# Performance work log

Measured on AMD Instinct MI355X. Metric: run time of the kernel, lower is better.

## Reference

```python
import jax, jax.numpy as jnp
import numpy as np
from jax.scipy.special import logsumexp, gammaln

B, T, D, K = 2048, 512, 64, 16  # num_sequences, max_length, data_dim (tones), hidden_dim per factor


def setup_inputs() -> dict:
    key = jax.random.key(0)
    k0, k1, k2, k3, k4 = jax.random.split(key, 5)
    sequences = jax.random.randint(k0, (B, T, D), 0, 2).astype(jnp.int32)  # binary piano-roll obs
    lengths = jax.random.randint(k1, (B,), 1, T + 1).astype(jnp.int32)
    probs_w = jax.nn.softmax(jax.random.normal(k2, (K, K), dtype=jnp.float32), axis=-1)  # row-stochastic
    probs_x = jax.nn.softmax(jax.random.normal(k3, (K, K), dtype=jnp.float32), axis=-1)
    probs_y = jax.random.uniform(k4, (K, K, D), dtype=jnp.float32) * 0.98 + 0.01  # in (0.01, 0.99)
    return {"sequences": sequences, "lengths": lengths,
            "probs_w": probs_w, "probs_x": probs_x, "probs_y": probs_y}


def _dirichlet_logpdf_rows(p, conc):
    # sum over rows of Dirichlet(conc_row).log_prob(p_row)
    return (((conc - 1.0) * jnp.log(p)).sum()
            + gammaln(conc.sum(-1)).sum() - gammaln(conc).sum())


def _log_joint(sequences, lengths, probs_w, probs_x, probs_y):
    dt = probs_y.dtype
    logTw = jnp.log(probs_w)            # (K, K) transition for w factor
    logTx = jnp.log(probs_x)            # (K, K) transition for x factor
    lp = jnp.log(probs_y)               # (K, K, D)
    l1p = jnp.log1p(-probs_y)           # (K, K, D)
    Wemit = (lp - l1p).reshape(K * K, D)        # Bernoulli log-odds per joint state
    base = l1p.sum(-1).reshape(K * K)           # sum_d log(1-p)

    ys = jnp.swapaxes(sequences, 0, 1)          # (T, B, D) int
    mask = jnp.arange(T)[:, None] < lengths[None, :]  # (T, B)

    # alpha[b, w, x]: forward log-prob; initial deterministic state (w, x) = (0, 0)
    alpha0 = jnp.full((B, K, K), -1e9, dtype=dt).at[:, 0, 0].set(0.0)

    def step(alpha, inp):
        y_t, m_t = inp
        y_f = y_t.astype(dt)                                    # (B, D)
        logE = (y_f @ Wemit.T + base).reshape(B, K, K)          # emission log-prob per (w', x')
        # marginalize previous w: (B, x, w')
        tmp = logsumexp(alpha[:, :, :, None] + logTw[None, :, None, :], axis=1)
        # marginalize previous x: (B, w', x')
        new = logsumexp(tmp[:, :, :, None] + logTx[None, :, None, :], axis=1)
        new = new + logE
        alpha = jnp.where(m_t[:, None, None], new, alpha)       # frozen past sequence end
        return alpha, None

    alpha, _ = jax.lax.scan(step, alpha0, (ys, mask))
    seq_ll = logsumexp(alpha.reshape(B, K * K), axis=-1)        # (B,) marginal log-likelihood

    # priors: Dirichlet(0.9*I + 0.1) on transition rows, Beta(0.1, 0.9) on probs_y
    conc = 0.9 * jnp.eye(K, dtype=dt) + 0.1
    prior = _dirichlet_logpdf_rows(probs_w, conc) + _dirichlet_logpdf_rows(probs_x, conc)
    a, b = 0.1, 0.9
    log_beta_norm = gammaln(a) + gammaln(b) - gammaln(a + b)
    prior = prior + ((a - 1.0) * lp + (b - 1.0) * l1p).sum() - log_beta_norm * (K * K * D)

    return seq_ll.sum() + prior


def reference(sequences, lengths, probs_w, probs_x, probs_y):
    return _log_joint(sequences, lengths, probs_w, probs_x, probs_y)
```

## Files before the change

### kernel.cpp

```cpp
#include <hip/hip_runtime.h>
#include <math.h>

#define NB 2048
#define NT 512
#define ND 64

typedef float    f32x4 __attribute__((ext_vector_type(4)));
typedef short    s16x8 __attribute__((ext_vector_type(8)));

#define MFMA32(A,B,C) __builtin_amdgcn_mfma_f32_16x16x32_bf16((A),(B),(C),0,0,0)

#if __has_builtin(__builtin_amdgcn_exp2f)
#define EXP2F(x) __builtin_amdgcn_exp2f(x)
#else
#define EXP2F(x) __expf((x) * 0.6931471805599453f)
#endif
#if __has_builtin(__builtin_amdgcn_logf)
#define LOG2F(x) __builtin_amdgcn_logf(x)
#else
#define LOG2F(x) (__logf(x) * 1.4426950408889634f)
#endif
#if __has_builtin(__builtin_amdgcn_rcpf)
#define RCPF(x) __builtin_amdgcn_rcpf(x)
#else
#define RCPF(x) __fdividef(1.0f, (x))
#endif

__device__ __forceinline__ unsigned short bf16rn(float f) {
  unsigned u = __float_as_uint(f);
  unsigned r = u + 0x7FFFu + ((u >> 16) & 1u);
  return (unsigned short)(r >> 16);
}
__device__ __forceinline__ unsigned pack2(float a, float b) {
  return (unsigned)bf16rn(a) | ((unsigned)bf16rn(b) << 16);
}
__device__ __forceinline__ unsigned pack2t(float a, float b) {
  return (__float_as_uint(a) >> 16) | (__float_as_uint(b) & 0xFFFF0000u);
}

union frag8 { s16x8 s8; unsigned u[4]; };

__device__ __forceinline__ s16x8 pack8t(f32x4 x) {
  frag8 r;
  r.u[0] = pack2t(x[0], x[1]);
  r.u[1] = pack2t(x[2], x[3]);
  r.u[2] = 0u; r.u[3] = 0u;
  return r.s8;
}

__global__ void fhmm_init(const float* __restrict__ py,
                          unsigned short* __restrict__ ws16,
                          float* __restrict__ partials)
{
  const float LOG2E = 1.4426950408889634f;
  int t = blockIdx.x * 256 + threadIdx.x;
  if (t < 2048) partials[t] = 0.f;
  if (t < 2048) {
    int st = t >> 7, kk = (t >> 6) & 1, l = t & 63;
    int rho = st * 16 + (l & 15);
    int s = (4 * (rho >> 6) + (rho & 3)) * 16 + ((rho >> 2) & 15);
    int d0 = kk * 32 + 8 * (l >> 4);
    unsigned short* dst = ws16 + (size_t)t * 8;
#pragma unroll
    for (int i = 0; i < 8; ++i) {
      float p = py[s * 64 + d0 + i];
      dst[i] = bf16rn((logf(p) - log1pf(-p)) * LOG2E);
    }
  } else if (t < 3072) {
    int t2 = t - 2048;
    int st = t2 >> 6, l = t2 & 63;
    unsigned short v[8] = {0, 0, 0, 0, 0, 0, 0, 0};
    if (l < 16) {
      int rho = st * 16 + l;
      int s = (4 * (rho >> 6) + (rho & 3)) * 16 + ((rho >> 2) & 15);
      float base = 0.f;
      for (int d = 0; d < 64; ++d) base += log1pf(-py[s * 64 + d]);
      base *= LOG2E;
      unsigned short hi = bf16rn(base);
      float basehi = __uint_as_float(((unsigned)hi) << 16);
      v[0] = hi;
      v[1] = bf16rn(base - basehi);
    }
    unsigned short* dst = ws16 + (size_t)(2048 + t2) * 8;
#pragma unroll
    for (int i = 0; i < 8; ++i) dst[i] = v[i];
  }
}

__global__ void fhmm_sort(const int* __restrict__ lengths, int* __restrict__ perm)
{
  __shared__ int hist[512];
  __shared__ int cnt[512];
  __shared__ int sa[512], sb2[512];
  const int tid = threadIdx.x;
  hist[tid] = 0; hist[tid + 256] = 0;
  cnt[tid] = 0;  cnt[tid + 256] = 0;
  __syncthreads();
  int myb[8];
#pragma unroll
  for (int u = 0; u < 8; ++u) {
    int i = tid + 256 * u;
    myb[u] = 512 - lengths[i];
    atomicAdd(&hist[myb[u]], 1);
  }
  __syncthreads();
  sa[tid] = hist[tid]; sa[tid + 256] = hist[tid + 256];
  __syncthreads();
  int* src = sa; int* dst = sb2;
  for (int off = 1; off < 512; off <<= 1) {
    for (int k = tid; k < 512; k += 256)
      dst[k] = src[k] + ((k >= off) ? src[k - off] : 0);
    __syncthreads();
    int* tp = src; src = dst; dst = tp;
  }
#pragma unroll
  for (int u = 0; u < 8; ++u) {
    int i = tid + 256 * u;
    int b2 = myb[u];
    int pos = src[b2] - hist[b2] + atomicAdd(&cnt[b2], 1);
    perm[pos] = i;
  }
}

__global__ __launch_bounds__(256, 2) void fhmm_fwd2(
    const int* __restrict__ seq, const int* __restrict__ lengths,
    const float* __restrict__ pw, const float* __restrict__ px,
    const void* __restrict__ wfrag, const int* __restrict__ perm,
    float* __restrict__ partials)
{
  __shared__ f32x4 e_lds[4][1024];

  const int tid = threadIdx.x;
  const int wv = tid >> 6, j = tid & 63;
  const int q = j >> 4, tl = j & 15;
  const int bid = blockIdx.x;
  const int lb  = (bid < 256) ? bid : (767 - bid);
  const int b = perm[(lb << 2) | wv];
  if (b < 0 || b >= NB) return;
  f32x4* e_w = e_lds[wv];
  const s16x8* wf_g = (const s16x8*)wfrag;
  const s16x8* w2_g = wf_g + 2048;

  s16x8 twb8, txb8;
  {
    frag8 a, c;
    a.u[0] = pack2(pw[(4 * q + 0) * 16 + tl], pw[(4 * q + 1) * 16 + tl]);
    a.u[1] = pack2(pw[(4 * q + 2) * 16 + tl], pw[(4 * q + 3) * 16 + tl]);
    a.u[2] = 0u; a.u[3] = 0u;
    c.u[0] = pack2(px[(4 * q + 0) * 16 + tl], px[(4 * q + 1) * 16 + tl]);
    c.u[1] = pack2(px[(4 * q + 2) * 16 + tl], px[(4 * q + 3) * 16 + tl]);
    c.u[2] = 0u; c.u[3] = 0u;
    twb8 = a.s8; txb8 = c.s8;
  }

  s16x8 f2 = {0, 0, 0, 0, 0, 0, 0, 0};
  if (q == 0) { f2[0] = (short)0x3F80; f2[1] = (short)0x3F80; }

  s16x8 ones8;
  {
    frag8 o;
    o.u[0] = 0x3F803F80u; o.u[1] = 0x3F803F80u;
    o.u[2] = 0x3F803F80u; o.u[3] = 0x3F803F80u;
    ones8 = o.s8;
  }

  f32x4 p = {0.f, 0.f, 0.f, 0.f};
  if (j == 0) p[0] = 1.f;

  const int len = lengths[b];
  const int* ybase = seq + (size_t)b * NT * ND;

  int4 ya0, ya1, yb0, yb1;
  {
    const int* yr = ybase + (size_t)tl * ND + 8 * q;
    const int4* pp  = (const int4*)yr;
    const int4* pp2 = (const int4*)(yr + 32);
    ya0 = pp[0]; ya1 = pp[1]; yb0 = pp2[0]; yb1 = pp2[1];
  }

  float L2 = 0.f, Ls = 0.f, R = 0.f;
  const f32x4 z4 = {0.f, 0.f, 0.f, 0.f};

  for (int t0 = 0; t0 < len; t0 += 16) {
    union { s16x8 s; unsigned u[4]; } f0u, f1u;
    f0u.u[0] = (ya0.x ? 0x3F80u : 0u) | (ya0.y ? 0x3F800000u : 0u);
    f0u.u[1] = (ya0.z ? 0x3F80u : 0u) | (ya0.w ? 0x3F800000u : 0u);
    f0u.u[2] = (ya1.x ? 0x3F80u : 0u) | (ya1.y ? 0x3F800000u : 0u);
    f0u.u[3] = (ya1.z ? 0x3F80u : 0u) | (ya1.w ? 0x3F800000u : 0u);
    f1u.u[0] = (yb0.x ? 0x3F80u : 0u) | (yb0.y ? 0x3F800000u : 0u);
    f1u.u[1] = (yb0.z ? 0x3F80u : 0u) | (yb0.w ? 0x3F800000u : 0u);
    f1u.u[2] = (yb1.x ? 0x3F80u : 0u) | (yb1.y ? 0x3F800000u : 0u);
    f1u.u[3] = (yb1.z ? 0x3F80u : 0u) | (yb1.w ? 0x3F800000u : 0u);
    const s16x8 f0 = f0u.s, f1 = f1u.s;

    if (t0 + 16 < len) {
      const int* yr = ybase + (size_t)(t0 + 16 + tl) * ND + 8 * q;
      const int4* pp  = (const int4*)yr;
      const int4* pp2 = (const int4*)(yr + 32);
      ya0 = pp[0]; ya1 = pp[1]; yb0 = pp2[0]; yb1 = pp2[1];
    }

#pragma unroll
    for (int st = 0; st < 16; ++st) {
      f32x4 acc = MFMA32(w2_g[st * 64 + j], f2, z4);
      acc = MFMA32(wf_g[(2 * st + 0) * 64 + j], f0, acc);
      acc = MFMA32(wf_g[(2 * st + 1) * 64 + j], f1, acc);
      f32x4 G;
      G[0] = EXP2F(fminf(acc[0] - R, 80.f));
      G[1] = EXP2F(fminf(acc[1] - R, 80.f));
      G[2] = EXP2F(fminf(acc[2] - R, 80.f));
      G[3] = EXP2F(fminf(acc[3] - R, 80.f));
      e_w[tl * 64 + ((st * 4 + q) ^ tl)] = G;
    }

    const int nsteps = (len - t0 < 16) ? (len - t0) : 16;
    float LsC = 0.f;
    f32x4 gv = e_w[j];
    for (int it = 0; it < nsteps; ++it) {
      const f32x4 g = gv;
      const int itn = (it + 1) & 15;
      gv = e_w[itn * 64 + (j ^ itn)];
      s16x8 vb = pack8t(p);
      f32x4 P  = MFMA32(vb, twb8, z4);
      f32x4 S1 = MFMA32(vb, ones8, z4);
      f32x4 U  = MFMA32(pack8t(P), txb8, z4);
      f32x4 S2 = MFMA32(pack8t(S1), ones8, z4);
      const float s   = fmaxf(S2[0], 1e-30f);
      const float inv = RCPF(s);
      LsC += LOG2F(s);
      f32x4 pn;
      pn[0] = (U[0] * inv) * g[0];
      pn[1] = (U[1] * inv) * g[1];
      pn[2] = (U[2] * inv) * g[2];
      pn[3] = (U[3] * inv) * g[3];
      p = pn;
    }
    L2 += (float)nsteps * R;
    Ls += LsC;
    R  += LsC * 0.0625f;
  }
  {
    f32x4 F1 = MFMA32(pack8t(p), ones8, z4);
    f32x4 F2 = MFMA32(pack8t(F1), ones8, z4);
    float sf = fmaxf(F2[0], 1e-35f);
    float L = (L2 + Ls + LOG2F(sf)) * 0.6931471805599453f;
    if (j == 0) partials[b] = L;
  }
}

__global__ __launch_bounds__(256, 3) void fhmm_fwd1(
    const int* __restrict__ seq, const int* __restrict__ lengths,
    const float* __restrict__ pw, const float* __restrict__ px,
    const float* __restrict__ py, float* __restrict__ partials,
    float* __restrict__ out)
{
  const int b = blockIdx.x, tid = threadIdx.x;
  const int wp = tid >> 4, xc = tid & 15;
  float Twc[16], Txc[16], W[64], base = 0.f;
#pragma unroll
  for (int w = 0; w < 16; ++w) Twc[w] = pw[w * 16 + wp];
#pragma unroll
  for (int x = 0; x < 16; ++x) Txc[x] = px[x * 16 + xc];
#pragma unroll
  for (int d = 0; d < 64; ++d) {
    float pv = py[tid * 64 + d];
    W[d] = logf(pv) - log1pf(-pv);
    base += log1pf(-pv);
  }
  __shared__ __align__(16) float yf[64];
  __shared__ __align__(16) float v_s[256];
  __shared__ __align__(16) float tmp_s[256];
  __shared__ float red[8];
  const int len = lengths[b];
  const int* yb = seq + (size_t)b * (NT * ND);
  v_s[tid] = (tid == 0) ? 1.f : 0.f;
  float L = 0.f, ynext = 0.f;
  if (tid < 64) ynext = (float)yb[tid];
  for (int t = 0; t < len; ++t) {
    if (tid < 64) yf[tid] = ynext;
    __syncthreads();
    if (tid < 64 && (t + 1) < len) ynext = (float)yb[(t + 1) * ND + tid];
    float e0 = base, e1 = 0.f, e2 = 0.f, e3 = 0.f;
    const float4* y4p = (const float4*)yf;
#pragma unroll
    for (int i = 0; i < 16; ++i) {
      float4 y4 = y4p[i];
      e0 = fmaf(y4.x, W[4 * i + 0], e0); e1 = fmaf(y4.y, W[4 * i + 1], e1);
      e2 = fmaf(y4.z, W[4 * i + 2], e2); e3 = fmaf(y4.w, W[4 * i + 3], e3);
    }
    float e = (e0 + e1) + (e2 + e3);
    float s1a = 0.f, s1b = 0.f;
#pragma unroll
    for (int w = 0; w < 16; w += 2) {
      s1a = fmaf(Twc[w], v_s[w * 16 + xc], s1a);
      s1b = fmaf(Twc[w + 1], v_s[(w + 1) * 16 + xc], s1b);
    }
    tmp_s[tid] = s1a + s1b;
    float mm = e;
#pragma unroll
    for (int off = 32; off; off >>= 1) mm = fmaxf(mm, __shfl_xor(mm, off));
    if ((tid & 63) == 0) red[tid >> 6] = mm;
    __syncthreads();
    mm = fmaxf(fmaxf(red[0], red[1]), fmaxf(red[2], red[3]));
    float q0 = 0.f, q1 = 0.f;
    const float4* t4p = (const float4*)(tmp_s + wp * 16);
#pragma unroll
    for (int i = 0; i < 4; ++i) {
      float4 t4 = t4p[i];
      q0 = fmaf(t4.x, Txc[4 * i + 0], q0); q1 = fmaf(t4.y, Txc[4 * i + 1], q1);
      q0 = fmaf(t4.z, Txc[4 * i + 2], q0); q1 = fmaf(t4.w, Txc[4 * i + 3], q1);
    }
    float val = (q0 + q1) * __expf(e - mm);
    float s = val;
#pragma unroll
    for (int off = 32; off; off >>= 1) s += __shfl_xor(s, off);
    if ((tid & 63) == 0) red[4 + (tid >> 6)] = s;
    __syncthreads();
    s = (red[4] + red[5]) + (red[6] + red[7]);
    L += __logf(s) + mm;
    v_s[tid] = val * (1.0f / s);
  }
  if (partials) { if (tid == 0) partials[b] = L; }
  else { if (tid == 0) atomicAdd(out, L); }
}

__global__ void fhmm_finalize(const float* __restrict__ partials,
                              const float* __restrict__ pw,
                              const float* __restrict__ px,
                              const float* __restrict__ py,
                              float* __restrict__ out)
{
  const int tid = threadIdx.x;
  float a = 0.f;
  if (partials) {
#pragma unroll
    for (int i = 0; i < 8; ++i) a += partials[tid + 256 * i];
  }
  {
    int i = tid >> 4, j = tid & 15;
    if (i != j) a += -0.9f * (logf(pw[tid]) + logf(px[tid]));
  }
  for (int k = 0; k < 64; ++k) {
    float p = py[tid * 64 + k];
    a += -0.9f * logf(p) - 0.1f * log1pf(-p);
  }
  __shared__ float red[256];
  red[tid] = a;
  __syncthreads();
  for (int s = 128; s > 0; s >>= 1) {
    if (tid < s) red[tid] += red[tid + s];
    __syncthreads();
  }
  if (tid == 0) {
    const float cst =
        2.f * (16.f * 0.2846828704729192f - 240.f * 2.2527126517342055f)
        - (2.2527126517342055f + 0.0663762397347443f) * 16384.f;
    out[0] = red[0] + cst;
  }
}

extern "C" void kernel_launch(void* const* d_in, const int* in_sizes, int n_in,
                              void* d_out, int out_size, void* d_ws, size_t ws_size,
                              hipStream_t stream) {
  const int*   seq = (const int*)d_in[0];
  const int*   len = (const int*)d_in[1];
  const float* pw  = (const float*)d_in[2];
  const float* px  = (const float*)d_in[3];
  const float* py  = (const float*)d_in[4];
  float*       out = (float*)d_out;

  const size_t NEED = 65536;
  if (ws_size >= NEED) {
    unsigned short* wf = (unsigned short*)d_ws;
    float* partials = (float*)((char*)d_ws + 49152);
    int*   perm     = (int*)((char*)d_ws + 57344);
    fhmm_init<<<12, 256, 0, stream>>>(py, wf, partials);
    fhmm_sort<<<1, 256, 0, stream>>>(len, perm);
    fhmm_fwd2<<<512, 256, 0, stream>>>(seq, len, pw, px, (const void*)wf, perm, partials);
    fhmm_finalize<<<1, 256, 0, stream>>>(partials, pw, px, py, out);
  } else if (ws_size >= 2048 * sizeof(float)) {
    float* partials = (float*)d_ws;
    fhmm_fwd1<<<NB, 256, 0, stream>>>(seq, len, pw, px, py, partials, out);
    fhmm_finalize<<<1, 256, 0, stream>>>(partials, pw, px, py, out);
  } else {
    fhmm_finalize<<<1, 256, 0, stream>>>(nullptr, pw, px, py, out);
    fhmm_fwd1<<<NB, 256, 0, stream>>>(seq, len, pw, px, py, nullptr, out);
  }
}
```

Baseline: 206.8 us.

## Interleave two sequences per wavefront to hide serial MFMA dependency latency

Each wavefront now runs the forward recursion for two length-sorted sequences at once, interleaving their dependent MFMA chains step by step so one sequence's latency overlaps the other's work. The grid is halved to 256 blocks with launch bounds of one block per CU, and the per-wave emission LDS buffer is doubled. It also drops the previous serpentine block-to-length mapping and clamps the prefetch row at the sequence end. The cost is higher register and LDS pressure and less occupancy, and paired sequences with different lengths leave some steps idle.

Measured after the change: 415.3 us. 101% more time.

```diff
diff --git a/kernel.cpp b/kernel.cpp
--- a/kernel.cpp
+++ b/kernel.cpp
@@ -122,22 +122,23 @@
   }
 }
 
-__global__ __launch_bounds__(256, 2) void fhmm_fwd2(
-    const int* __restrict__ seq, const int* __restrict__ lengths,
+__global__ __launch_bounds__(256, 1) void fhmm_fwd2(
+    const int* __restrict__ seqg, const int* __restrict__ lengths,
     const float* __restrict__ pw, const float* __restrict__ px,
     const void* __restrict__ wfrag, const int* __restrict__ perm,
     float* __restrict__ partials)
 {
-  __shared__ f32x4 e_lds[4][1024];
+  __shared__ f32x4 e_lds[4][2][1024];
 
   const int tid = threadIdx.x;
   const int wv = tid >> 6, j = tid & 63;
   const int q = j >> 4, tl = j & 15;
-  const int bid = blockIdx.x;
-  const int lb  = (bid < 256) ? bid : (767 - bid);
-  const int b = perm[(lb << 2) | wv];
-  if (b < 0 || b >= NB) return;
-  f32x4* e_w = e_lds[wv];
+  const int pi = (blockIdx.x << 2) | wv;
+  const int bA = perm[2 * pi];
+  const int bB = perm[2 * pi + 1];
+  if (bA < 0 || bA >= NB || bB < 0 || bB >= NB) return;
+  f32x4* eA = e_lds[wv][0];
+  f32x4* eB = e_lds[wv][1];
   const s16x8* wf_g = (const s16x8*)wfrag;
   const s16x8* w2_g = wf_g + 2048;
 
@@ -164,88 +165,138 @@
     ones8 = o.s8;
   }
 
-  f32x4 p = {0.f, 0.f, 0.f, 0.f};
-  if (j == 0) p[0] = 1.f;
-
-  const int len = lengths[b];
-  const int* ybase = seq + (size_t)b * NT * ND;
-
-  int4 ya0, ya1, yb0, yb1;
+  const int lenA = lengths[bA];
+  const int lenB = lengths[bB];
+  const int* ybaseA = seqg + (size_t)bA * NT * ND;
+  const int* ybaseB = seqg + (size_t)bB * NT * ND;
+  const f32x4 z4 = {0.f, 0.f, 0.f, 0.f};
+
+  f32x4 pA = z4, pB = z4;
+  if (j == 0) { pA[0] = 1.f; pB[0] = 1.f; }
+
+  int4 ya0A, ya1A, yb0A, yb1A, ya0B, ya1B, yb0B, yb1B;
+  s16x8 f0A, f1A, f0B, f1B;
+  f32x4 gvA, gvB;
+
+#define LOADY(S, ROWBASE)                                                  \
+  {                                                                        \
+    int row_ = (ROWBASE) + tl;                                             \
+    if (row_ > len##S - 1) row_ = len##S - 1;         \
+    const int* yr_ = ybase##S + (size_t)row_ * ND + 8 * q;                 \
+    ya0##S = ((const int4*)yr_)[0];                                        \
+    ya1##S = ((const int4*)yr_)[1];                                        \
+    yb0##S = ((const int4*)(yr_ + 32))[0];                                 \
+    yb1##S = ((const int4*)(yr_ + 32))[1];                                 \
+  }
+
+#define BUILDF(S)                                                          \
+  {                                                                        \
+    frag8 f0u_, f1u_;                                                      \
+    f0u_.u[0] = (ya0##S.x ? 0x3F80u : 0u) | (ya0##S.y ? 0x3F800000u : 0u); \
+    f0u_.u[1] = (ya0##S.z ? 0x3F80u : 0u) | (ya0##S.w ? 0x3F800000u : 0u); \
+    f0u_.u[2] = (ya1##S.x ? 0x3F80u : 0u) | (ya1##S.y ? 0x3F800000u : 0u); \
+    f0u_.u[3] = (ya1##S.z ? 0x3F80u : 0u) | (ya1##S.w ? 0x3F800000u : 0u); \
+    f1u_.u[0] = (yb0##S.x ? 0x3F80u : 0u) | (yb0##S.y ? 0x3F800000u : 0u); \
+    f1u_.u[1] = (yb0##S.z ? 0x3F80u : 0u) | (yb0##S.w ? 0x3F800000u : 0u); \
+    f1u_.u[2] = (yb1##S.x ? 0x3F80u : 0u) | (yb1##S.y ? 0x3F800000u : 0u); \
+    f1u_.u[3] = (yb1##S.z ? 0x3F80u : 0u) | (yb1##S.w ? 0x3F800000u : 0u); \
+    f0##S = f0u_.s8; f1##S = f1u_.s8;                                      \
+  }
+
+#define EMIT16(S, EO)                                                      \
+  {                                                                        \
+    _Pragma("unroll")                                                      \
+    for (int st = 0; st < 16; ++st) {                                      \
+      f32x4 acc_ = MFMA32(w2_g[st * 64 + j], f2, z4);                      \
+      acc_ = MFMA32(wf_g[(2 * st + 0) * 64 + j], f0##S, acc_);             \
+      acc_ = MFMA32(wf_g[(2 * st + 1) * 64 + j], f1##S, acc_);             \
+      f32x4 G_;                                                            \
+      G_[0] = EXP2F(fminf(acc_[0] - R##S, 80.f));                          \
+      G_[1] = EXP2F(fminf(acc_[1] - R##S, 80.f));                          \
+      G_[2] = EXP2F(fminf(acc_[2] - R##S, 80.f));                          \
+      G_[3] = EXP2F(fminf(acc_[3] - R##S, 80.f));                          \
+      (EO)[tl * 64 + ((st * 4 + q) ^ tl)] = G_;                            \
+    }                                                                      \
+  }
+
+#define STEP(S, IT, EO)                                                    \
+  {                                                                        \
+    const f32x4 g_ = gv##S;                                                \
+    const int itn_ = ((IT) + 1) & 15;                                      \
+    gv##S = (EO)[itn_ * 64 + (j ^ itn_)];                                  \
+    s16x8 vb_ = pack8t(p##S);                                              \
+    f32x4 P_  = MFMA32(vb_, twb8, z4);                                     \
+    f32x4 S1_ = MFMA32(vb_, ones8, z4);                                    \
+    f32x4 U_  = MFMA32(pack8t(P_), txb8, z4);                              \
+    f32x4 S2_ = MFMA32(pack8t(S1_), ones8, z4);                            \
+    const float s_   = fmaxf(S2_[0], 1e-30f);                              \
+    const float inv_ = RCPF(s_);                                           \
+    Ls##S += LOG2F(s_);                                                    \
+    p##S[0] = (U_[0] * inv_) * g_[0];                                      \
+    p##S[1] = (U_[1] * inv_) * g_[1];                                      \
+    p##S[2] = (U_[2] * inv_) * g_[2];                                      \
+    p##S[3] = (U_[3] * inv_) * g_[3];                                      \
+  }
+
+  LOADY(A, 0)
+  LOADY(B, 0)
+
+  float L2A = 0.f, LsA = 0.f, RA = 0.f;
+  float L2B = 0.f, LsB = 0.f, RB = 0.f;
+
+  for (int t0 = 0; t0 < lenA; t0 += 16) {
+    const int nsA = (lenA - t0 < 16) ? (lenA - t0) : 16;
+    int nsB = lenB - t0;
+    nsB = (nsB < 0) ? 0 : ((nsB > 16) ? 16 : nsB);
+
+    BUILDF(A)
+    if (nsB > 0) BUILDF(B)
+    if (t0 + 16 < lenA) LOADY(A, t0 + 16)
+    if (t0 + 16 < lenB) LOADY(B, t0 + 16)
+
+    EMIT16(A, eA)
+    if (nsB > 0) EMIT16(B, eB)
+
+    const float Ls0A = LsA, Ls0B = LsB;
+    gvA = eA[j];
+    gvB = eB[j];
+    if (nsA == 16 && nsB == 16) {
+#define DSTEP(IT) { STEP(A, IT, eA) STEP(B, IT, eB) }
+      DSTEP(0)  DSTEP(1)  DSTEP(2)  DSTEP(3)
+      DSTEP(4)  DSTEP(5)  DSTEP(6)  DSTEP(7)
+      DSTEP(8)  DSTEP(9)  DSTEP(10) DSTEP(11)
+      DSTEP(12) DSTEP(13) DSTEP(14) DSTEP(15)
+#undef DSTEP
+    } else {
+      for (int it = 0; it < 16; ++it) {
+        if (it < nsA) STEP(A, it, eA)
+        if (it < nsB) STEP(B, it, eB)
+      }
+    }
+    L2A += (float)nsA * RA;
+    RA  += (LsA - Ls0A) * 0.0625f;
+    L2B += (float)nsB * RB;
+    RB  += (LsB - Ls0B) * 0.0625f;
+  }
+
   {
-    const int* yr = ybase + (size_t)tl * ND + 8 * q;
-    const int4* pp  = (const int4*)yr;
-    const int4* pp2 = (const int4*)(yr + 32);
-    ya0 = pp[0]; ya1 = pp[1]; yb0 = pp2[0]; yb1 = pp2[1];
-  }
-
-  float L2 = 0.f, Ls = 0.f, R = 0.f;
-  const f32x4 z4 = {0.f, 0.f, 0.f, 0.f};
-
-  for (int t0 = 0; t0 < len; t0 += 16) {
-    union { s16x8 s; unsigned u[4]; } f0u, f1u;
-    f0u.u[0] = (ya0.x ? 0x3F80u : 0u) | (ya0.y ? 0x3F800000u : 0u);
-    f0u.u[1] = (ya0.z ? 0x3F80u : 0u) | (ya0.w ? 0x3F800000u : 0u);
-    f0u.u[2] = (ya1.x ? 0x3F80u : 0u) | (ya1.y ? 0x3F800000u : 0u);
-    f0u.u[3] = (ya1.z ? 0x3F80u : 0u) | (ya1.w ? 0x3F800000u : 0u);
-    f1u.u[0] = (yb0.x ? 0x3F80u : 0u) | (yb0.y ? 0x3F800000u : 0u);
-    f1u.u[1] = (yb0.z ? 0x3F80u : 0u) | (yb0.w ? 0x3F800000u : 0u);
-    f1u.u[2] = (yb1.x ? 0x3F80u : 0u) | (yb1.y ? 0x3F800000u : 0u);
-    f1u.u[3] = (yb1.z ? 0x3F80u : 0u) | (yb1.w ? 0x3F800000u : 0u);
-    const s16x8 f0 = f0u.s, f1 = f1u.s;
-
-    if (t0 + 16 < len) {
-      const int* yr = ybase + (size_t)(t0 + 16 + tl) * ND + 8 * q;
-      const int4* pp  = (const int4*)yr;
-      const int4* pp2 = (const int4*)(yr + 32);
-      ya0 = pp[0]; ya1 = pp[1]; yb0 = pp2[0]; yb1 = pp2[1];
-    }
-
-#pragma unroll
-    for (int st = 0; st < 16; ++st) {
-      f32x4 acc = MFMA32(w2_g[st * 64 + j], f2, z4);
-      acc = MFMA32(wf_g[(2 * st + 0) * 64 + j], f0, acc);
-      acc = MFMA32(wf_g[(2 * st + 1) * 64 + j], f1, acc);
-      f32x4 G;
-      G[0] = EXP2F(fminf(acc[0] - R, 80.f));
-      G[1] = EXP2F(fminf(acc[1] - R, 80.f));
-      G[2] = EXP2F(fminf(acc[2] - R, 80.f));
-      G[3] = EXP2F(fminf(acc[3] - R, 80.f));
-      e_w[tl * 64 + ((st * 4 + q) ^ tl)] = G;
-    }
-
-    const int nsteps = (len - t0 < 16) ? (len - t0) : 16;
-    float LsC = 0.f;
-    f32x4 gv = e_w[j];
-    for (int it = 0; it < nsteps; ++it) {
-      const f32x4 g = gv;
-      const int itn = (it + 1) & 15;
-      gv = e_w[itn * 64 + (j ^ itn)];
-      s16x8 vb = pack8t(p);
-      f32x4 P  = MFMA32(vb, twb8, z4);
-      f32x4 S1 = MFMA32(vb, ones8, z4);
-      f32x4 U  = MFMA32(pack8t(P), txb8, z4);
-      f32x4 S2 = MFMA32(pack8t(S1), ones8, z4);
-      const float s   = fmaxf(S2[0], 1e-30f);
-      const float inv = RCPF(s);
-      LsC += LOG2F(s);
-      f32x4 pn;
-      pn[0] = (U[0] * inv) * g[0];
-      pn[1] = (U[1] * inv) * g[1];
-      pn[2] = (U[2] * inv) * g[2];
-      pn[3] = (U[3] * inv) * g[3];
-      p = pn;
-    }
-    L2 += (float)nsteps * R;
-    Ls += LsC;
-    R  += LsC * 0.0625f;
-  }
-  {
-    f32x4 F1 = MFMA32(pack8t(p), ones8, z4);
+    f32x4 F1 = MFMA32(pack8t(pA), ones8, z4);
     f32x4 F2 = MFMA32(pack8t(F1), ones8, z4);
     float sf = fmaxf(F2[0], 1e-35f);
-    float L = (L2 + Ls + LOG2F(sf)) * 0.6931471805599453f;
-    if (j == 0) partials[b] = L;
-  }
+    float L = (L2A + LsA + LOG2F(sf)) * 0.6931471805599453f;
+    if (j == 0) partials[bA] = L;
+  }
+  {
+    f32x4 F1 = MFMA32(pack8t(pB), ones8, z4);
+    f32x4 F2 = MFMA32(pack8t(F1), ones8, z4);
+    float sf = fmaxf(F2[0], 1e-35f);
+    float L = (L2B + LsB + LOG2F(sf)) * 0.6931471805599453f;
+    if (j == 0) partials[bB] = L;
+  }
+#undef LOADY
+#undef BUILDF
+#undef EMIT16
+#undef STEP
 }
 
 __global__ __launch_bounds__(256, 3) void fhmm_fwd1(
@@ -376,7 +427,7 @@
     int*   perm     = (int*)((char*)d_ws + 57344);
     fhmm_init<<<12, 256, 0, stream>>>(py, wf, partials);
     fhmm_sort<<<1, 256, 0, stream>>>(len, perm);
-    fhmm_fwd2<<<512, 256, 0, stream>>>(seq, len, pw, px, (const void*)wf, perm, partials);
+    fhmm_fwd2<<<256, 256, 0, stream>>>(seq, len, pw, px, (const void*)wf, perm, partials);
     fhmm_finalize<<<1, 256, 0, stream>>>(partials, pw, px, py, out);
   } else if (ws_size >= 2048 * sizeof(float)) {
     float* partials = (float*)d_ws;
```
